# Optimization experiments

Hardware: AMD Instinct MI355X
Metric: run time of the kernel (lower is better)

The kernel has to match this reference:

```python
import jax, jax.numpy as jnp
import numpy as np

N_NODES = 50000
N_EDGES = 800000
D = 64
HID = 256


def setup_inputs() -> dict:
    key = jax.random.key(0)
    ks = jax.random.split(key, 6)
    nodes = jax.random.normal(ks[0], (N_NODES, D), dtype=jnp.float32)
    edges = jax.random.normal(ks[1], (N_EDGES, D), dtype=jnp.float32)
    senders = jax.random.randint(ks[2], (N_EDGES,), 0, N_NODES, dtype=jnp.int32)
    receivers = jax.random.randint(ks[3], (N_EDGES,), 0, N_NODES, dtype=jnp.int32)
    W1 = jax.random.normal(ks[4], (2 * D, HID), dtype=jnp.float32) * (1.0 / np.sqrt(2 * D))
    b1 = jnp.zeros((HID,), dtype=jnp.float32)
    W2 = jax.random.normal(ks[5], (HID, D), dtype=jnp.float32) * (1.0 / np.sqrt(HID))
    b2 = jnp.zeros((D,), dtype=jnp.float32)
    return {"nodes": nodes, "edges": edges, "senders": senders,
            "receivers": receivers, "W1": W1, "b1": b1, "W2": W2, "b2": b2}


def reference(nodes, edges, senders, receivers, W1, b1, W2, b2):
    # EdgesToNodesAggregator: scatter-sum edges by senders PLUS by receivers -> [N, d_edge]
    agg = (jax.ops.segment_sum(edges, senders, num_segments=N_NODES)
           + jax.ops.segment_sum(edges, receivers, num_segments=N_NODES))
    collected = jnp.concatenate([agg, nodes], axis=-1)  # [N, d_edge + d_node]
    h = jax.nn.relu(collected @ W1 + b1)                # [N, HID]
    updated_nodes = h @ W2 + b2                         # [N, D]
    return updated_nodes
```

## Files before the change

### kernel.cpp

```cpp
#include <hip/hip_runtime.h>
#include <hip/hip_bf16.h>

#define N_NODES 50000
#define N_EDGES 800000
#define D       64
#define HID     256
#define DIN     128
#define NB      32

#define MB1     64
#define KC1     32
#define MB2     64
#define KC2     32

__global__ __launch_bounds__(256) void degree_kernel(
    const int* __restrict__ senders,
    const int* __restrict__ receivers,
    int* __restrict__ deg)
{
    int e = blockIdx.x * 256 + threadIdx.x;
    if (e < N_EDGES) {
        atomicAdd(&deg[senders[e]],   1);
        atomicAdd(&deg[receivers[e]], 1);
    }
}

__global__ __launch_bounds__(256) void scan_bsum_kernel(
    const int* __restrict__ deg, int* __restrict__ bsum)
{
    __shared__ int ws[4];
    const int t = threadIdx.x;
    const int i4 = blockIdx.x * 256 + t;
    int s = 0;
    if (i4 < N_NODES / 4) {
        int4 dv = reinterpret_cast<const int4*>(deg)[i4];
        s = dv.x + dv.y + dv.z + dv.w;
    }
    #pragma unroll
    for (int off = 32; off; off >>= 1) s += __shfl_down(s, off, 64);
    if ((t & 63) == 0) ws[t >> 6] = s;
    __syncthreads();
    if (t == 0) bsum[blockIdx.x] = ws[0] + ws[1] + ws[2] + ws[3];
}

__global__ __launch_bounds__(64) void scan_boff_kernel(
    const int* __restrict__ bsum, int* __restrict__ boff,
    int* __restrict__ offs_last, int nblocks)
{
    const int t = threadIdx.x;
    int v = (t < nblocks) ? bsum[t] : 0;
    int x = v;
    #pragma unroll
    for (int off = 1; off < 64; off <<= 1) {
        int y = __shfl_up(x, off, 64);
        if (t >= off) x += y;
    }
    if (t < nblocks) boff[t] = x - v;
    if (t == nblocks - 1) offs_last[0] = x;
}

__global__ __launch_bounds__(256) void scan_write_kernel(
    const int* __restrict__ deg, const int* __restrict__ boff,
    int* __restrict__ offs, int* __restrict__ cursor)
{
    __shared__ int wsum[4];
    const int t = threadIdx.x, lane = t & 63, w = t >> 6;
    const int i4 = blockIdx.x * 256 + t;
    int4 dv = make_int4(0, 0, 0, 0);
    if (i4 < N_NODES / 4) dv = reinterpret_cast<const int4*>(deg)[i4];
    const int s = dv.x + dv.y + dv.z + dv.w;
    int x = s;
    #pragma unroll
    for (int off = 1; off < 64; off <<= 1) {
        int y = __shfl_up(x, off, 64);
        if (lane >= off) x += y;
    }
    if (lane == 63) wsum[w] = x;
    __syncthreads();
    int wpre = 0;
    #pragma unroll
    for (int i = 0; i < 4; ++i) if (i < w) wpre += wsum[i];
    const int base = boff[blockIdx.x] + wpre + (x - s);
    int4 o;
    o.x = base; o.y = base + dv.x; o.z = o.y + dv.y; o.w = o.z + dv.z;
    if (i4 < N_NODES / 4) {
        reinterpret_cast<int4*>(offs)[i4]   = o;
        reinterpret_cast<int4*>(cursor)[i4] = o;
    }
}

__global__ __launch_bounds__(256) void fill_kernel(
    const int* __restrict__ senders,
    const int* __restrict__ receivers,
    int* __restrict__ cursor,
    int* __restrict__ eidx)
{
    int e = blockIdx.x * 256 + threadIdx.x;
    if (e < N_EDGES) {
        int p = atomicAdd(&cursor[senders[e]],   1); eidx[p] = e;
        int q = atomicAdd(&cursor[receivers[e]], 1); eidx[q] = e;
    }
}

__global__ __launch_bounds__(256) void gather_kernel(
    const float* __restrict__ edges,
    const int* __restrict__ offs,
    const int* __restrict__ eidx,
    float* __restrict__ agg)
{
    const int node = blockIdx.x * 4 + (threadIdx.x >> 6);
    const int lane = threadIdx.x & 63;
    if (node >= N_NODES) return;

    const int beg = offs[node], end = offs[node + 1];
    float a0 = 0.f, a1 = 0.f;
    int i = beg;
    for (; i + 8 <= end; i += 8) {
        int e0 = eidx[i],   e1 = eidx[i+1], e2 = eidx[i+2], e3 = eidx[i+3];
        int e4 = eidx[i+4], e5 = eidx[i+5], e6 = eidx[i+6], e7 = eidx[i+7];
        float v0 = edges[(size_t)e0 * D + lane];
        float v1 = edges[(size_t)e1 * D + lane];
        float v2 = edges[(size_t)e2 * D + lane];
        float v3 = edges[(size_t)e3 * D + lane];
        float v4 = edges[(size_t)e4 * D + lane];
        float v5 = edges[(size_t)e5 * D + lane];
        float v6 = edges[(size_t)e6 * D + lane];
        float v7 = edges[(size_t)e7 * D + lane];
        a0 += (v0 + v1) + (v2 + v3);
        a1 += (v4 + v5) + (v6 + v7);
    }
    for (; i < end; ++i) a0 += edges[(size_t)eidx[i] * D + lane];
    agg[(size_t)node * D + lane] = a0 + a1;
}

__global__ __launch_bounds__(256, 2) void gemm1_kernel(
    const float* __restrict__ agg,
    const float* __restrict__ nodes,
    const float* __restrict__ W1,
    const float* __restrict__ b1,
    float* __restrict__ hbuf)
{
    __shared__ __align__(16) float xs[MB1][DIN + 4];
    __shared__ __align__(16) float wls[KC1][HID];

    const int t = threadIdx.x;
    const int node0 = blockIdx.x * MB1;
    const int gn = t >> 5;
    const int gj = t & 31;

    for (int f = t; f < MB1 * 32; f += 256) {
        int n = f >> 5, c = f & 31;
        int node = node0 + n;
        float4 v = make_float4(0.f, 0.f, 0.f, 0.f);
        if (node < N_NODES)
            v = (c < 16) ? reinterpret_cast<const float4*>(agg   + (size_t)node * D)[c]
                         : reinterpret_cast<const float4*>(nodes + (size_t)node * D)[c - 16];
        *reinterpret_cast<float4*>(&xs[n][c * 4]) = v;
    }

    float acc[8][8];
    #pragma unroll
    for (int i = 0; i < 8; ++i)
        #pragma unroll
        for (int c = 0; c < 8; ++c) acc[i][c] = 0.f;

    for (int kc = 0; kc < DIN; kc += KC1) {
        __syncthreads();
        for (int f = t; f < KC1 * 64; f += 256) {
            int kk = f >> 6, c = f & 63;
            *reinterpret_cast<float4*>(&wls[kk][c * 4]) =
                reinterpret_cast<const float4*>(W1 + (size_t)(kc + kk) * HID)[c];
        }
        __syncthreads();

        #pragma unroll
        for (int k4 = 0; k4 < KC1; k4 += 4) {
            float4 xv[8];
            #pragma unroll
            for (int i = 0; i < 8; ++i)
                xv[i] = *reinterpret_cast<const float4*>(&xs[8 * gn + i][kc + k4]);
            float wv[4][8];
            #pragma unroll
            for (int kk = 0; kk < 4; ++kk)
                #pragma unroll
                for (int c = 0; c < 8; ++c) wv[kk][c] = wls[k4 + kk][gj + 32 * c];
            #pragma unroll
            for (int i = 0; i < 8; ++i)
                #pragma unroll
                for (int c = 0; c < 8; ++c) {
                    acc[i][c] = fmaf(xv[i].x, wv[0][c], acc[i][c]);
                    acc[i][c] = fmaf(xv[i].y, wv[1][c], acc[i][c]);
                    acc[i][c] = fmaf(xv[i].z, wv[2][c], acc[i][c]);
                    acc[i][c] = fmaf(xv[i].w, wv[3][c], acc[i][c]);
                }
        }
    }

    float bb[8];
    #pragma unroll
    for (int c = 0; c < 8; ++c) bb[c] = b1[gj + 32 * c];
    #pragma unroll
    for (int i = 0; i < 8; ++i) {
        const int node = node0 + 8 * gn + i;
        if (node < N_NODES) {
            #pragma unroll
            for (int c = 0; c < 8; ++c)
                hbuf[(size_t)node * HID + gj + 32 * c] = fmaxf(acc[i][c] + bb[c], 0.f);
        }
    }
}

__global__ __launch_bounds__(256, 4) void gemm2_kernel(
    const float* __restrict__ hbuf,
    const float* __restrict__ W2,
    const float* __restrict__ b2,
    float* __restrict__ out)
{
    __shared__ __align__(16) float hs[MB2][KC2 + 4];
    __shared__ __align__(16) float w2s[KC2][D + 4];

    const int t = threadIdx.x;
    const int node0 = blockIdx.x * MB2;
    const int tn = t >> 4;
    const int td = t & 15;

    float acc[4][4];
    #pragma unroll
    for (int i = 0; i < 4; ++i)
        #pragma unroll
        for (int j = 0; j < 4; ++j) acc[i][j] = 0.f;

    for (int kc = 0; kc < HID; kc += KC2) {
        __syncthreads();
        for (int f = t; f < MB2 * 8; f += 256) {
            int n = f >> 3, c = f & 7;
            int node = node0 + n;
            float4 v = make_float4(0.f, 0.f, 0.f, 0.f);
            if (node < N_NODES)
                v = reinterpret_cast<const float4*>(hbuf + (size_t)node * HID + kc)[c];
            *reinterpret_cast<float4*>(&hs[n][c * 4]) = v;
        }
        for (int f = t; f < KC2 * 16; f += 256) {
            int kk = f >> 4, c = f & 15;
            *reinterpret_cast<float4*>(&w2s[kk][c * 4]) =
                reinterpret_cast<const float4*>(W2 + (size_t)(kc + kk) * D)[c];
        }
        __syncthreads();

        #pragma unroll
        for (int k4 = 0; k4 < KC2; k4 += 4) {
            float4 hv[4];
            #pragma unroll
            for (int i = 0; i < 4; ++i)
                hv[i] = *reinterpret_cast<const float4*>(&hs[4 * tn + i][k4]);
            float4 wv[4];
            #pragma unroll
            for (int kk = 0; kk < 4; ++kk)
                wv[kk] = *reinterpret_cast<const float4*>(&w2s[k4 + kk][4 * td]);
            #pragma unroll
            for (int i = 0; i < 4; ++i) {
                acc[i][0] = fmaf(hv[i].x, wv[0].x, acc[i][0]);
                acc[i][1] = fmaf(hv[i].x, wv[0].y, acc[i][1]);
                acc[i][2] = fmaf(hv[i].x, wv[0].z, acc[i][2]);
                acc[i][3] = fmaf(hv[i].x, wv[0].w, acc[i][3]);
                acc[i][0] = fmaf(hv[i].y, wv[1].x, acc[i][0]);
                acc[i][1] = fmaf(hv[i].y, wv[1].y, acc[i][1]);
                acc[i][2] = fmaf(hv[i].y, wv[1].z, acc[i][2]);
                acc[i][3] = fmaf(hv[i].y, wv[1].w, acc[i][3]);
                acc[i][0] = fmaf(hv[i].z, wv[2].x, acc[i][0]);
                acc[i][1] = fmaf(hv[i].z, wv[2].y, acc[i][1]);
                acc[i][2] = fmaf(hv[i].z, wv[2].z, acc[i][2]);
                acc[i][3] = fmaf(hv[i].z, wv[2].w, acc[i][3]);
                acc[i][0] = fmaf(hv[i].w, wv[3].x, acc[i][0]);
                acc[i][1] = fmaf(hv[i].w, wv[3].y, acc[i][1]);
                acc[i][2] = fmaf(hv[i].w, wv[3].z, acc[i][2]);
                acc[i][3] = fmaf(hv[i].w, wv[3].w, acc[i][3]);
            }
        }
    }

    const float4 bb = *reinterpret_cast<const float4*>(b2 + 4 * td);
    #pragma unroll
    for (int i = 0; i < 4; ++i) {
        const int node = node0 + 4 * tn + i;
        if (node < N_NODES) {
            float4 o = make_float4(acc[i][0] + bb.x, acc[i][1] + bb.y,
                                   acc[i][2] + bb.z, acc[i][3] + bb.w);
            reinterpret_cast<float4*>(out + (size_t)node * D)[td] = o;
        }
    }
}

__global__ __launch_bounds__(256) void scatter_kernel(
    const float* __restrict__ edges,
    const int* __restrict__ senders,
    const int* __restrict__ receivers,
    float* __restrict__ agg)
{
    int tid = blockIdx.x * 256 + threadIdx.x;
    int e = tid >> 4;
    int c = (tid & 15) << 2;
    if (e >= N_EDGES) return;
    const float4 v = *reinterpret_cast<const float4*>(edges + (long)e * D + c);
    int s = senders[e] * D + c;
    int r = receivers[e] * D + c;
    atomicAdd(&agg[s + 0], v.x); atomicAdd(&agg[s + 1], v.y);
    atomicAdd(&agg[s + 2], v.z); atomicAdd(&agg[s + 3], v.w);
    atomicAdd(&agg[r + 0], v.x); atomicAdd(&agg[r + 1], v.y);
    atomicAdd(&agg[r + 2], v.z); atomicAdd(&agg[r + 3], v.w);
}

__global__ __launch_bounds__(256, 2) void mlp_kernel(
    const float* __restrict__ agg, const float* __restrict__ nodes,
    const float* __restrict__ W1, const float* __restrict__ b1,
    const float* __restrict__ W2, const float* __restrict__ b2,
    float* __restrict__ out)
{
    __shared__ __align__(16) float x_lds[NB][DIN];
    __shared__ __align__(16) float h_lds[NB][HID];
    const int t = threadIdx.x;
    const int node0 = blockIdx.x * NB;

    for (int f = t; f < NB * DIN / 4; f += 256) {
        int n = f >> 5, c = f & 31;
        int node = node0 + n;
        float4 v = make_float4(0.f, 0.f, 0.f, 0.f);
        if (node < N_NODES) {
            const float* src = (c < 16) ? (agg   + (size_t)node * D + c * 4)
                                        : (nodes + (size_t)node * D + (c - 16) * 4);
            v = *reinterpret_cast<const float4*>(src);
        }
        *reinterpret_cast<float4*>(&x_lds[n][c * 4]) = v;
    }
    float w1c[DIN];
    #pragma unroll
    for (int k = 0; k < DIN; ++k) w1c[k] = W1[(size_t)k * HID + t];
    const float bias1 = b1[t];
    __syncthreads();

    for (int n = 0; n < NB; ++n) {
        const float4* xr = reinterpret_cast<const float4*>(x_lds[n]);
        float a0 = 0.f, a1 = 0.f, a2 = 0.f, a3 = 0.f;
        #pragma unroll
        for (int k4 = 0; k4 < 32; ++k4) {
            float4 x = xr[k4];
            a0 = fmaf(w1c[4*k4 + 0], x.x, a0);
            a1 = fmaf(w1c[4*k4 + 1], x.y, a1);
            a2 = fmaf(w1c[4*k4 + 2], x.z, a2);
            a3 = fmaf(w1c[4*k4 + 3], x.w, a3);
        }
        h_lds[n][t] = fmaxf(bias1 + ((a0 + a1) + (a2 + a3)), 0.0f);
    }
    __syncthreads();

    const int d  = t & 63;
    const int ng = t >> 6;
    float acc2[8];
    #pragma unroll
    for (int i = 0; i < 8; ++i) acc2[i] = 0.0f;
    for (int j = 0; j < HID; j += 4) {
        const float w0 = W2[(j + 0) * D + d];
        const float w1 = W2[(j + 1) * D + d];
        const float w2 = W2[(j + 2) * D + d];
        const float w3 = W2[(j + 3) * D + d];
        #pragma unroll
        for (int i = 0; i < 8; ++i) {
            const int n = ng + 4 * i;
            const float4 h4 = *reinterpret_cast<const float4*>(&h_lds[n][j]);
            acc2[i] = fmaf(w0, h4.x, acc2[i]);
            acc2[i] = fmaf(w1, h4.y, acc2[i]);
            acc2[i] = fmaf(w2, h4.z, acc2[i]);
            acc2[i] = fmaf(w3, h4.w, acc2[i]);
        }
    }
    const float bias2 = b2[d];
    #pragma unroll
    for (int i = 0; i < 8; ++i) {
        const int n = ng + 4 * i;
        const int node = node0 + n;
        if (node < N_NODES) out[(size_t)node * D + d] = acc2[i] + bias2;
    }
}

extern "C" void kernel_launch(void* const* d_in, const int* in_sizes, int n_in,
                              void* d_out, int out_size, void* d_ws, size_t ws_size,
                              hipStream_t stream)
{
    const float* nodes     = (const float*)d_in[0];
    const float* edges     = (const float*)d_in[1];
    const int*   senders   = (const int*)  d_in[2];
    const int*   receivers = (const int*)  d_in[3];
    const float* W1        = (const float*)d_in[4];
    const float* b1        = (const float*)d_in[5];
    const float* W2        = (const float*)d_in[6];
    const float* b2        = (const float*)d_in[7];
    float* out = (float*)d_out;

    float* agg    = (float*)d_ws;
    int*   deg    = (int*)d_ws + 3200000;
    int*   offs   = deg + 50000;
    int*   cursor = offs + 50004;
    int*   eidx   = cursor + 50000;
    int*   bsum   = eidx + 1600000;
    int*   boff   = bsum + 64;
    float* hbuf   = (float*)(boff + 64);
    const size_t csr_bytes  = (3200000 + 50000 + 50004 + 50000 + 1600000 + 128) * 4ull;
    const size_t full_bytes = csr_bytes + 12800000ull * 4ull;

    const int eb = (N_EDGES + 255) / 256;
    const int sb = (N_NODES / 4 + 255) / 256;
    const int gemm_blocks = (N_NODES + MB1 - 1) / MB1;

    if (ws_size >= csr_bytes) {
        hipMemsetAsync(deg, 0, N_NODES * sizeof(int), stream);
        degree_kernel<<<eb, 256, 0, stream>>>(senders, receivers, deg);
        scan_bsum_kernel<<<sb, 256, 0, stream>>>(deg, bsum);
        scan_boff_kernel<<<1, 64, 0, stream>>>(bsum, boff, &offs[N_NODES], sb);
        scan_write_kernel<<<sb, 256, 0, stream>>>(deg, boff, offs, cursor);
        fill_kernel<<<eb, 256, 0, stream>>>(senders, receivers, cursor, eidx);
        gather_kernel<<<(N_NODES + 3) / 4, 256, 0, stream>>>(edges, offs, eidx, agg);

        if (ws_size >= full_bytes) {
            gemm1_kernel<<<gemm_blocks, 256, 0, stream>>>(agg, nodes, W1, b1, hbuf);
            gemm2_kernel<<<gemm_blocks, 256, 0, stream>>>(hbuf, W2, b2, out);
        } else {
            mlp_kernel<<<(N_NODES + NB - 1) / NB, 256, 0, stream>>>(
                agg, nodes, W1, b1, W2, b2, out);
        }
    } else {
        hipMemsetAsync(agg, 0, (size_t)N_NODES * D * sizeof(float), stream);
        scatter_kernel<<<(N_EDGES * 16) / 256, 256, 0, stream>>>(edges, senders, receivers, agg);
        mlp_kernel<<<(N_NODES + NB - 1) / NB, 256, 0, stream>>>(
            agg, nodes, W1, b1, W2, b2, out);
    }
}
```

Measured before the change: 663.8 us.

## Replace CSR build and gather with range-partitioned shared-memory edge aggregation

Drops the degree count, three-stage scan, CSR fill and gather kernels. Each block now owns a 448-node range and scans a quarter of the edge list, compacting matching sender/receiver hits into a per-wave shared queue. It then accumulates the edge rows into a shared-memory tile with LDS atomics. A separate reduce kernel sums the four slice partials, and the hidden buffer reuses the partials workspace. This removes the global atomics and the multiple passes of CSR construction, at the cost of every block re-reading the full sender/receiver index arrays and holding a large shared-memory footprint that allows one block per CU.

```diff
diff --git a/kernel.cpp b/kernel.cpp
--- a/kernel.cpp
+++ b/kernel.cpp
@@ -13,124 +13,123 @@
 #define MB2     64
 #define KC2     32
 
-__global__ __launch_bounds__(256) void degree_kernel(
+#define NR          448
+#define NRANGE      ((N_NODES + NR - 1) / NR)
+#define NSLICE      4
+#define SLICE_E     ((N_EDGES + NSLICE - 1) / NSLICE)
+#define QCAP        1024
+#define AGG_THREADS 512
+
+__global__ __launch_bounds__(AGG_THREADS, 1) void agg_kernel(
+    const float* __restrict__ edges,
     const int* __restrict__ senders,
     const int* __restrict__ receivers,
-    int* __restrict__ deg)
-{
-    int e = blockIdx.x * 256 + threadIdx.x;
-    if (e < N_EDGES) {
-        atomicAdd(&deg[senders[e]],   1);
-        atomicAdd(&deg[receivers[e]], 1);
-    }
-}
-
-__global__ __launch_bounds__(256) void scan_bsum_kernel(
-    const int* __restrict__ deg, int* __restrict__ bsum)
-{
-    __shared__ int ws[4];
-    const int t = threadIdx.x;
-    const int i4 = blockIdx.x * 256 + t;
-    int s = 0;
-    if (i4 < N_NODES / 4) {
-        int4 dv = reinterpret_cast<const int4*>(deg)[i4];
-        s = dv.x + dv.y + dv.z + dv.w;
-    }
-    #pragma unroll
-    for (int off = 32; off; off >>= 1) s += __shfl_down(s, off, 64);
-    if ((t & 63) == 0) ws[t >> 6] = s;
+    float* __restrict__ partials)
+{
+    __shared__ float sagg[(NR + 1) * D];
+    __shared__ unsigned int squeue[8 * QCAP];
+
+    const int t     = threadIdx.x;
+    const int lane  = t & 63;
+    const int wid   = t >> 6;
+    const int range = blockIdx.x / NSLICE;
+    const int slice = blockIdx.x % NSLICE;
+    const int node0 = range * NR;
+    const int ebeg  = slice * SLICE_E;
+    const int eend  = min(N_EDGES, ebeg + SLICE_E);
+
+    for (int i = t; i < NR * (D / 4); i += AGG_THREADS)
+        reinterpret_cast<float4*>(sagg)[i] = make_float4(0.f, 0.f, 0.f, 0.f);
     __syncthreads();
-    if (t == 0) bsum[blockIdx.x] = ws[0] + ws[1] + ws[2] + ws[3];
-}
-
-__global__ __launch_bounds__(64) void scan_boff_kernel(
-    const int* __restrict__ bsum, int* __restrict__ boff,
-    int* __restrict__ offs_last, int nblocks)
-{
-    const int t = threadIdx.x;
-    int v = (t < nblocks) ? bsum[t] : 0;
-    int x = v;
-    #pragma unroll
-    for (int off = 1; off < 64; off <<= 1) {
-        int y = __shfl_up(x, off, 64);
-        if (t >= off) x += y;
-    }
-    if (t < nblocks) boff[t] = x - v;
-    if (t == nblocks - 1) offs_last[0] = x;
-}
-
-__global__ __launch_bounds__(256) void scan_write_kernel(
-    const int* __restrict__ deg, const int* __restrict__ boff,
-    int* __restrict__ offs, int* __restrict__ cursor)
-{
-    __shared__ int wsum[4];
-    const int t = threadIdx.x, lane = t & 63, w = t >> 6;
-    const int i4 = blockIdx.x * 256 + t;
-    int4 dv = make_int4(0, 0, 0, 0);
-    if (i4 < N_NODES / 4) dv = reinterpret_cast<const int4*>(deg)[i4];
-    const int s = dv.x + dv.y + dv.z + dv.w;
-    int x = s;
-    #pragma unroll
-    for (int off = 1; off < 64; off <<= 1) {
-        int y = __shfl_up(x, off, 64);
-        if (lane >= off) x += y;
-    }
-    if (lane == 63) wsum[w] = x;
+
+    unsigned int* wq = &squeue[wid * QCAP];
+    int qcnt = 0;
+
+    auto drain_all = [&]() {
+        const int padded = (qcnt + 7) & ~7;
+        if (lane < padded - qcnt)
+            wq[qcnt + lane] = (0u << 10) | (unsigned)NR;
+        for (int k = 0; k < padded; k += 8) {
+            unsigned a[8]; float v[8];
+            #pragma unroll
+            for (int u = 0; u < 8; ++u) a[u] = wq[k + u];
+            #pragma unroll
+            for (int u = 0; u < 8; ++u)
+                v[u] = edges[(size_t)(a[u] >> 10) * D + lane];
+            #pragma unroll
+            for (int u = 0; u < 8; ++u)
+                atomicAdd(&sagg[(a[u] & 1023u) * D + lane], v[u]);
+        }
+        qcnt = 0;
+    };
+
+    const int nchunks = (eend - ebeg + 64 * 8 - 1) / (64 * 8);
+    for (int i = 0; i < nchunks; i += 8) {
+        int sv[8], rv[8], ix[8];
+        #pragma unroll
+        for (int u = 0; u < 8; ++u) {
+            const int idx = ebeg + (wid + 8 * (i + u)) * 64 + lane;
+            ix[u] = idx;
+            const bool ok = idx < eend;
+            sv[u] = ok ? senders[idx]   : 0x7fffffff;
+            rv[u] = ok ? receivers[idx] : 0x7fffffff;
+        }
+        #pragma unroll
+        for (int u = 0; u < 8; ++u) {
+            {
+                const unsigned ln = (unsigned)(sv[u] - node0);
+                const bool hit = ln < (unsigned)NR;
+                const unsigned long long m = __ballot(hit);
+                if (hit) {
+                    const int pos = qcnt + __popcll(m & ((1ull << lane) - 1ull));
+                    wq[pos] = ((unsigned)ix[u] << 10) | ln;
+                }
+                qcnt += __popcll(m);
+            }
+            {
+                const unsigned ln = (unsigned)(rv[u] - node0);
+                const bool hit = ln < (unsigned)NR;
+                const unsigned long long m = __ballot(hit);
+                if (hit) {
+                    const int pos = qcnt + __popcll(m & ((1ull << lane) - 1ull));
+                    wq[pos] = ((unsigned)ix[u] << 10) | ln;
+                }
+                qcnt += __popcll(m);
+            }
+            if (qcnt >= QCAP - 128) drain_all();
+        }
+    }
+    drain_all();
     __syncthreads();
-    int wpre = 0;
-    #pragma unroll
-    for (int i = 0; i < 4; ++i) if (i < w) wpre += wsum[i];
-    const int base = boff[blockIdx.x] + wpre + (x - s);
-    int4 o;
-    o.x = base; o.y = base + dv.x; o.z = o.y + dv.y; o.w = o.z + dv.z;
-    if (i4 < N_NODES / 4) {
-        reinterpret_cast<int4*>(offs)[i4]   = o;
-        reinterpret_cast<int4*>(cursor)[i4] = o;
-    }
-}
-
-__global__ __launch_bounds__(256) void fill_kernel(
-    const int* __restrict__ senders,
-    const int* __restrict__ receivers,
-    int* __restrict__ cursor,
-    int* __restrict__ eidx)
-{
-    int e = blockIdx.x * 256 + threadIdx.x;
-    if (e < N_EDGES) {
-        int p = atomicAdd(&cursor[senders[e]],   1); eidx[p] = e;
-        int q = atomicAdd(&cursor[receivers[e]], 1); eidx[q] = e;
-    }
-}
-
-__global__ __launch_bounds__(256) void gather_kernel(
-    const float* __restrict__ edges,
-    const int* __restrict__ offs,
-    const int* __restrict__ eidx,
-    float* __restrict__ agg)
-{
-    const int node = blockIdx.x * 4 + (threadIdx.x >> 6);
-    const int lane = threadIdx.x & 63;
-    if (node >= N_NODES) return;
-
-    const int beg = offs[node], end = offs[node + 1];
-    float a0 = 0.f, a1 = 0.f;
-    int i = beg;
-    for (; i + 8 <= end; i += 8) {
-        int e0 = eidx[i],   e1 = eidx[i+1], e2 = eidx[i+2], e3 = eidx[i+3];
-        int e4 = eidx[i+4], e5 = eidx[i+5], e6 = eidx[i+6], e7 = eidx[i+7];
-        float v0 = edges[(size_t)e0 * D + lane];
-        float v1 = edges[(size_t)e1 * D + lane];
-        float v2 = edges[(size_t)e2 * D + lane];
-        float v3 = edges[(size_t)e3 * D + lane];
-        float v4 = edges[(size_t)e4 * D + lane];
-        float v5 = edges[(size_t)e5 * D + lane];
-        float v6 = edges[(size_t)e6 * D + lane];
-        float v7 = edges[(size_t)e7 * D + lane];
-        a0 += (v0 + v1) + (v2 + v3);
-        a1 += (v4 + v5) + (v6 + v7);
-    }
-    for (; i < end; ++i) a0 += edges[(size_t)eidx[i] * D + lane];
-    agg[(size_t)node * D + lane] = a0 + a1;
+
+    for (int i = t; i < NR * (D / 4); i += AGG_THREADS) {
+        const int row = i >> 4, c = i & 15;
+        const int node = node0 + row;
+        if (node < N_NODES) {
+            const float4 vv = *reinterpret_cast<const float4*>(&sagg[row * D + c * 4]);
+            reinterpret_cast<float4*>(partials)
+                [(size_t)slice * N_NODES * (D / 4) + (size_t)node * (D / 4) + c] = vv;
+        }
+    }
+}
+
+__global__ __launch_bounds__(256) void reduce_kernel(
+    const float4* __restrict__ p, float4* __restrict__ agg)
+{
+    const size_t NF4 = (size_t)N_NODES * (D / 4);
+    const size_t i = (size_t)blockIdx.x * 256 + threadIdx.x;
+    if (i < NF4) {
+        float4 a = p[i];
+        float4 b = p[i + NF4];
+        float4 c = p[i + 2 * NF4];
+        float4 d = p[i + 3 * NF4];
+        float4 o;
+        o.x = (a.x + b.x) + (c.x + d.x);
+        o.y = (a.y + b.y) + (c.y + d.y);
+        o.z = (a.z + b.z) + (c.z + d.z);
+        o.w = (a.w + b.w) + (c.w + d.w);
+        agg[i] = o;
+    }
 }
 
 __global__ __launch_bounds__(256, 2) void gemm1_kernel(
@@ -396,37 +395,21 @@
     const float* b2        = (const float*)d_in[7];
     float* out = (float*)d_out;
 
-    float* agg    = (float*)d_ws;
-    int*   deg    = (int*)d_ws + 3200000;
-    int*   offs   = deg + 50000;
-    int*   cursor = offs + 50004;
-    int*   eidx   = cursor + 50000;
-    int*   bsum   = eidx + 1600000;
-    int*   boff   = bsum + 64;
-    float* hbuf   = (float*)(boff + 64);
-    const size_t csr_bytes  = (3200000 + 50000 + 50004 + 50000 + 1600000 + 128) * 4ull;
-    const size_t full_bytes = csr_bytes + 12800000ull * 4ull;
-
-    const int eb = (N_EDGES + 255) / 256;
-    const int sb = (N_NODES / 4 + 255) / 256;
+    float* agg      = (float*)d_ws;
+    float* partials = agg + (size_t)N_NODES * D;
+    float* hbuf     = partials;
+    const size_t need_bytes =
+        ((size_t)N_NODES * D + (size_t)NSLICE * N_NODES * D) * sizeof(float);
+
     const int gemm_blocks = (N_NODES + MB1 - 1) / MB1;
 
-    if (ws_size >= csr_bytes) {
-        hipMemsetAsync(deg, 0, N_NODES * sizeof(int), stream);
-        degree_kernel<<<eb, 256, 0, stream>>>(senders, receivers, deg);
-        scan_bsum_kernel<<<sb, 256, 0, stream>>>(deg, bsum);
-        scan_boff_kernel<<<1, 64, 0, stream>>>(bsum, boff, &offs[N_NODES], sb);
-        scan_write_kernel<<<sb, 256, 0, stream>>>(deg, boff, offs, cursor);
-        fill_kernel<<<eb, 256, 0, stream>>>(senders, receivers, cursor, eidx);
-        gather_kernel<<<(N_NODES + 3) / 4, 256, 0, stream>>>(edges, offs, eidx, agg);
-
-        if (ws_size >= full_bytes) {
-            gemm1_kernel<<<gemm_blocks, 256, 0, stream>>>(agg, nodes, W1, b1, hbuf);
-            gemm2_kernel<<<gemm_blocks, 256, 0, stream>>>(hbuf, W2, b2, out);
-        } else {
-            mlp_kernel<<<(N_NODES + NB - 1) / NB, 256, 0, stream>>>(
-                agg, nodes, W1, b1, W2, b2, out);
-        }
+    if (ws_size >= need_bytes) {
+        agg_kernel<<<NRANGE * NSLICE, AGG_THREADS, 0, stream>>>(
+            edges, senders, receivers, partials);
+        reduce_kernel<<<(N_NODES * (D / 4) + 255) / 256, 256, 0, stream>>>(
+            (const float4*)partials, (float4*)agg);
+        gemm1_kernel<<<gemm_blocks, 256, 0, stream>>>(agg, nodes, W1, b1, hbuf);
+        gemm2_kernel<<<gemm_blocks, 256, 0, stream>>>(hbuf, W2, b2, out);
     } else {
         hipMemsetAsync(agg, 0, (size_t)N_NODES * D * sizeof(float), stream);
         scatter_kernel<<<(N_EDGES * 16) / 256, 256, 0, stream>>>(edges, senders, receivers, agg);
```

Result: slower. 1.075 ms (+61.9%).
